# Kernel optimization log

Hardware: AMD Instinct MI355X
Metric: run time of the kernel (lower is better)

The kernel has to match this reference:

```python
import jax, jax.numpy as jnp
import numpy as np

B, S, D, H, HD, NU, T = 64, 512, 256, 4, 64, 100000, 24


def setup_inputs() -> dict:
    key = jax.random.key(0)
    ks = jax.random.split(key, 13)
    return {
        "timeslot_embedded": jax.random.normal(ks[0], (T, D), jnp.float32),
        "user": jax.random.randint(ks[1], (B,), 0, NU, dtype=jnp.int64) if jax.config.jax_enable_x64 else jax.random.randint(ks[1], (B,), 0, NU, dtype=jnp.int32),
        "hour": jax.random.randint(ks[2], (B, S), 0, T, dtype=jnp.int32),
        "hour_mask": jax.random.randint(ks[3], (B, S, T), 0, 2, dtype=jnp.int32),
        "user_pref": jax.random.normal(ks[4], (NU, D), jnp.float32) * 0.02,
        "Wq": jax.random.normal(ks[5], (H, HD, 2 * D), jnp.float32) * 0.02,
        "bq": jnp.zeros((H, HD), jnp.float32),
        "Wk": jax.random.normal(ks[6], (H, HD, D), jnp.float32) * 0.02,
        "bk": jnp.zeros((H, HD), jnp.float32),
        "Wv": jax.random.normal(ks[7], (H, HD, D), jnp.float32) * 0.02,
        "bv": jnp.zeros((H, HD), jnp.float32),
        "Wu": jax.random.normal(ks[8], (D, D), jnp.float32) * 0.02,
        "bu": jnp.zeros((D,), jnp.float32),
    }


def reference(timeslot_embedded, user, hour, hour_mask, user_pref,
              Wq, bq, Wk, bk, Wv, bv, Wu, bu):
    b, s = hour.shape
    n = b * s
    # per-token features
    user_feat = jnp.broadcast_to(user_pref[user][:, None, :], (b, s, D)).reshape(n, D)
    time_feat = timeslot_embedded[hour.reshape(n)]          # [N, D]
    query = jnp.concatenate([user_feat, time_feat], axis=-1)  # [N, 2D]
    # all heads at once (equivalent to the per-head Linear loop)
    q = jnp.einsum('nd,hkd->nhk', query, Wq) + bq[None]               # [N, H, HD]
    k = jnp.einsum('td,hkd->htk', timeslot_embedded, Wk) + bk[:, None, :]  # [H, T, HD]
    v = jnp.einsum('td,hkd->htk', timeslot_embedded, Wv) + bv[:, None, :]  # [H, T, HD]
    scale = 1.0 / np.sqrt(HD).astype(np.float32)
    scores = jnp.einsum('nhk,htk->nht', q, k) * scale                 # [N, H, T]
    mask = hour_mask.reshape(n, T)[:, None, :]                        # [N, 1, T]
    scores = jnp.where(mask == 1, -jnp.inf, scores)
    attn = jax.nn.softmax(scores, axis=-1)
    out = jnp.einsum('nht,htk->nhk', attn, v).reshape(n, H * HD)      # concat heads
    out = out @ Wu.T + bu
    return out.reshape(b, s, D)
```

## Files before the change

### kernel.cpp

```cpp
#include <hip/hip_runtime.h>
#include <hip/hip_bf16.h>

#define QU_OFF   0
#define KK_OFF   16384
#define ET_OFF   22528
#define VWB_OFF  24832

typedef __attribute__((ext_vector_type(8))) short bf16x8;
typedef __attribute__((ext_vector_type(4))) float f32x4;
typedef __attribute__((ext_vector_type(4))) int   i32x4;

__device__ __forceinline__ unsigned short f2bf(float f) {
    unsigned u = __builtin_bit_cast(unsigned, f);
    return (unsigned short)((u + 0x7FFFu + ((u >> 16) & 1u)) >> 16);
}
__device__ __forceinline__ unsigned packbf(float a, float b) {
    return (unsigned)f2bf(a) | ((unsigned)f2bf(b) << 16);
}
__device__ __forceinline__ bf16x8 cvt8(float4 f0, float4 f1) {
    int4 v = make_int4(packbf(f0.x, f0.y), packbf(f0.z, f0.w),
                       packbf(f1.x, f1.y), packbf(f1.z, f1.w));
    return __builtin_bit_cast(bf16x8, v);
}
__device__ __forceinline__ float dot4(float4 a, float4 b, float s) {
    return fmaf(a.x, b.x, fmaf(a.y, b.y, fmaf(a.z, b.z, fmaf(a.w, b.w, s))));
}
__device__ __forceinline__ float dot4v(f32x4 a, f32x4 b, float s) {
    return fmaf(a[0], b[0], fmaf(a[1], b[1], fmaf(a[2], b[2], fmaf(a[3], b[3], s))));
}


__global__ __launch_bounds__(256) void precomp(
    const float* __restrict__ ts, const int* __restrict__ user,
    const float* __restrict__ user_pref,
    const float* __restrict__ Wq, const float* __restrict__ bq,
    const float* __restrict__ Wk, const float* __restrict__ bk,
    const float* __restrict__ Wv, const float* __restrict__ bv,
    const float* __restrict__ Wu, float* __restrict__ ws)
{
    __shared__ unsigned sA[4096];
    __shared__ float sM1[32 * 68];
    __shared__ float sM2[32 * 68];
    int tid = threadIdx.x, blk = blockIdx.x;
    int w = tid >> 6, l = tid & 63;
    int eo = (l >> 4) * 8;

    if (blk < 16) {
        int q = blk >> 2, co = (blk & 3) * 64, b0 = q * 16;
        for (int u = tid; u < 512; u += 256) {
            int r = u >> 5, e0 = (u & 31) * 8;
            const float* src = user_pref + (size_t)user[b0 + r] * 256 + e0;
            float4 f0 = *(const float4*)src, f1 = *(const float4*)(src + 4);
            unsigned* dst = &sA[(((e0 >> 5) * 2) * 64 + (r & 15) + 16 * ((e0 >> 3) & 3)) * 4];
            dst[0] = packbf(f0.x, f0.y); dst[1] = packbf(f0.z, f0.w);
            dst[2] = packbf(f1.x, f1.y); dst[3] = packbf(f1.z, f1.w);
        }
        __syncthreads();
        int col = co + w * 16 + (l & 15);
        float4 fb[8][2];
        #pragma unroll
        for (int kt = 0; kt < 8; ++kt) {
            const float* Bp = Wq + (size_t)col * 512 + kt * 32 + eo;
            fb[kt][0] = *(const float4*)Bp; fb[kt][1] = *(const float4*)(Bp + 4);
        }
        f32x4 acc = (f32x4)0.f;
        #pragma unroll
        for (int kt = 0; kt < 8; ++kt) {
            bf16x8 afr = __builtin_bit_cast(bf16x8, *(const int4*)&sA[((kt * 2) * 64 + l) * 4]);
            acc = __builtin_amdgcn_mfma_f32_16x16x32_bf16(afr, cvt8(fb[kt][0], fb[kt][1]), acc, 0, 0, 0);
        }
        int row = (l >> 4) * 4;
        #pragma unroll
        for (int r = 0; r < 4; ++r)
            ws[QU_OFF + (size_t)(b0 + row + r) * 256 + col] = acc[r];
        return;
    }

    for (int u = tid; u < 768; u += 256) {
        int r = u >> 5, e0 = (u & 31) * 8;
        const float* src = ts + r * 256 + e0;
        float4 f0 = *(const float4*)src, f1 = *(const float4*)(src + 4);
        unsigned* dst = &sA[(((e0 >> 5) * 2 + (r >> 4)) * 64 + (r & 15) + 16 * ((e0 >> 3) & 3)) * 4];
        dst[0] = packbf(f0.x, f0.y); dst[1] = packbf(f0.z, f0.w);
        dst[2] = packbf(f1.x, f1.y); dst[3] = packbf(f1.z, f1.w);
    }
    __syncthreads();

    if (blk < 20) {
        int h = blk - 16;
        int j = h * 64 + w * 16 + (l & 15);
        float4 fa[8][2], fc[8][2];
        #pragma unroll
        for (int kt = 0; kt < 8; ++kt) {
            const float* Bq = Wq + (size_t)j * 512 + 256 + kt * 32 + eo;
            const float* Bk = Wk + (size_t)j * 256 + kt * 32 + eo;
            fa[kt][0] = *(const float4*)Bq; fa[kt][1] = *(const float4*)(Bq + 4);
            fc[kt][0] = *(const float4*)Bk; fc[kt][1] = *(const float4*)(Bk + 4);
        }
        f32x4 aca[2] = {(f32x4)0.f, (f32x4)0.f};
        f32x4 acb[2] = {(f32x4)0.f, (f32x4)0.f};
        #pragma unroll
        for (int kt = 0; kt < 8; ++kt) {
            bf16x8 bq8 = cvt8(fa[kt][0], fa[kt][1]);
            bf16x8 bk8 = cvt8(fc[kt][0], fc[kt][1]);
            #pragma unroll
            for (int mt = 0; mt < 2; ++mt) {
                bf16x8 afr = __builtin_bit_cast(bf16x8, *(const int4*)&sA[((kt * 2 + mt) * 64 + l) * 4]);
                aca[mt] = __builtin_amdgcn_mfma_f32_16x16x32_bf16(afr, bq8, aca[mt], 0, 0, 0);
                acb[mt] = __builtin_amdgcn_mfma_f32_16x16x32_bf16(afr, bk8, acb[mt], 0, 0, 0);
            }
        }
        float bqv = bq[j], bkv = bk[j];
        int hd = w * 16 + (l & 15);
        #pragma unroll
        for (int mt = 0; mt < 2; ++mt) {
            int t0 = mt * 16 + (l >> 4) * 4;
            #pragma unroll
            for (int r = 0; r < 4; ++r) {
                int t = t0 + r;
                if (t < 24) {
                    sM1[t * 68 + hd] = aca[mt][r] + bqv;
                    float kv = acb[mt][r] + bkv;
                    sM2[t * 68 + hd] = kv;
                    ws[KK_OFF + (h * 24 + t) * 64 + hd] = kv;
                }
            }
        }
        __syncthreads();
        for (int u = tid; u < 576; u += 256) {
            int tp = u / 24, t = u - tp * 24;
            const float4* qp4 = (const float4*)&sM1[tp * 68];
            const float4* kp4 = (const float4*)&sM2[t * 68];
            float s = 0.f;
            #pragma unroll
            for (int i = 0; i < 16; ++i) s = dot4(qp4[i], kp4[i], s);
            ws[ET_OFF + tp * 96 + h * 24 + t] = expf(s * 0.125f);
        }
        return;
    }

    {
        int h = blk - 20;
        int jv = h * 64 + w * 16 + (l & 15);
        float4 fv[8][2];
        #pragma unroll
        for (int kt = 0; kt < 8; ++kt) {
            const float* Bv = Wv + (size_t)jv * 256 + kt * 32 + eo;
            fv[kt][0] = *(const float4*)Bv; fv[kt][1] = *(const float4*)(Bv + 4);
        }
        f32x4 acv[2] = {(f32x4)0.f, (f32x4)0.f};
        #pragma unroll
        for (int kt = 0; kt < 8; ++kt) {
            bf16x8 bv8 = cvt8(fv[kt][0], fv[kt][1]);
            #pragma unroll
            for (int mt = 0; mt < 2; ++mt) {
                bf16x8 afr = __builtin_bit_cast(bf16x8, *(const int4*)&sA[((kt * 2 + mt) * 64 + l) * 4]);
                acv[mt] = __builtin_amdgcn_mfma_f32_16x16x32_bf16(afr, bv8, acv[mt], 0, 0, 0);
            }
        }
        float bvv = bv[jv];
        int hd = w * 16 + (l & 15);
        #pragma unroll
        for (int mt = 0; mt < 2; ++mt) {
            int t0 = mt * 16 + (l >> 4) * 4;
            #pragma unroll
            for (int r = 0; r < 4; ++r)
                if (t0 + r < 24) sM1[(t0 + r) * 68 + hd] = acv[mt][r] + bvv;
        }
        __syncthreads();
        f32x4 ac2[2][4];
        #pragma unroll
        for (int mt = 0; mt < 2; ++mt)
            #pragma unroll
            for (int q = 0; q < 4; ++q) ac2[mt][q] = (f32x4)0.f;
        #pragma unroll
        for (int kt2 = 0; kt2 < 2; ++kt2) {
            int k0 = kt2 * 32 + eo;
            bf16x8 a2[2];
            #pragma unroll
            for (int mt = 0; mt < 2; ++mt) {
                int m = mt * 16 + (l & 15);
                float4 g0 = *(const float4*)&sM1[m * 68 + k0];
                float4 g1 = *(const float4*)&sM1[m * 68 + k0 + 4];
                a2[mt] = cvt8(g0, g1);
            }
            float4 fu[4][2];
            #pragma unroll
            for (int q = 0; q < 4; ++q) {
                int d = (w * 4 + q) * 16 + (l & 15);
                const float* Bu = Wu + (size_t)d * 256 + h * 64 + k0;
                fu[q][0] = *(const float4*)Bu; fu[q][1] = *(const float4*)(Bu + 4);
            }
            #pragma unroll
            for (int q = 0; q < 4; ++q) {
                bf16x8 bu8 = cvt8(fu[q][0], fu[q][1]);
                #pragma unroll
                for (int mt = 0; mt < 2; ++mt)
                    ac2[mt][q] = __builtin_amdgcn_mfma_f32_16x16x32_bf16(a2[mt], bu8, ac2[mt][q], 0, 0, 0);
            }
        }
        unsigned* vwb = (unsigned*)(ws + VWB_OFF);
        #pragma unroll
        for (int mt = 0; mt < 2; ++mt) {
            int t0 = mt * 16 + (l >> 4) * 4;
            if (t0 < 24) {
                #pragma unroll
                for (int q = 0; q < 4; ++q) {
                    int d = (w * 4 + q) * 16 + (l & 15);
                    #pragma unroll
                    for (int pp = 0; pp < 2; ++pp) {
                        int ht = h * 24 + t0 + pp * 2;
                        unsigned pk = packbf(ac2[mt][q][pp * 2], ac2[mt][q][pp * 2 + 1]);
                        int ktC = ht >> 5, ntC = d >> 4;
                        int lgC = (ht >> 3) & 3, jhC = (ht & 7) >> 1;
                        vwb[(ktC * 16 + ntC) * 256 + ((d & 15) + 16 * lgC) * 4 + jhC] = pk;
                    }
                }
            }
        }
    }
}

__global__ __launch_bounds__(512) void attn_mfma(
    const int* __restrict__ hour, const int* __restrict__ hour_mask,
    const float* __restrict__ ws, const float* __restrict__ bu,
    float* __restrict__ out)
{
    const float* ET = ws + ET_OFF;
    __shared__ int4 A_lds[24 * 64];
    __shared__ float EU_s[96];
    __shared__ __align__(16) float stg[8 * 1088];
    int tid = threadIdx.x, w = tid >> 6, l = tid & 63;
    int mh = w >> 2, ns = w & 3;
    int nb = blockIdx.x * 128;
    int b = nb >> 9;

    int tok = tid >> 2, h = tid & 3, n = nb + tok;
    int th = hour[n];
    const i32x4* mp = (const i32x4*)(hour_mask + (long long)n * 24);
    i32x4 msk[6];
    #pragma unroll
    for (int q = 0; q < 6; ++q) msk[q] = __builtin_nontemporal_load(mp + q);
    const int4* Bg = (const int4*)(ws + VWB_OFF);
    int4 breg[12];
    #pragma unroll
    for (int kt = 0; kt < 3; ++kt)
        #pragma unroll
        for (int q = 0; q < 4; ++q)
            breg[kt * 4 + q] = Bg[(kt * 16 + ns * 4 + q) * 64 + l];
    if (tid < 96) {
        const f32x4* qp = (const f32x4*)(ws + QU_OFF + b * 256 + (tid / 24) * 64);
        const f32x4* kp = (const f32x4*)(ws + KK_OFF + tid * 64);
        float s = 0.f;
        #pragma unroll
        for (int i = 0; i < 16; ++i) s = dot4v(qp[i], kp[i], s);
        EU_s[tid] = expf(s * 0.125f);
    }
    const f32x4* ETp = (const f32x4*)(ET + th * 96 + h * 24);
    f32x4 fET[6];
    #pragma unroll
    for (int q = 0; q < 6; ++q) fET[q] = ETp[q];
    __syncthreads();
    {
        const f32x4* EUp = (const f32x4*)(EU_s + h * 24);
        float p[24]; float ssum = 0.f;
        #pragma unroll
        for (int q = 0; q < 6; ++q) {
            f32x4 e = EUp[q]; f32x4 f = fET[q]; i32x4 mm = msk[q];
            float v0 = (mm[0] != 0) ? 0.f : e[0] * f[0];
            float v1 = (mm[1] != 0) ? 0.f : e[1] * f[1];
            float v2 = (mm[2] != 0) ? 0.f : e[2] * f[2];
            float v3 = (mm[3] != 0) ? 0.f : e[3] * f[3];
            p[q*4+0] = v0; p[q*4+1] = v1; p[q*4+2] = v2; p[q*4+3] = v3;
            ssum += (v0 + v1) + (v2 + v3);
        }
        float r = 1.0f / ssum;
        int mt8 = tok >> 4, tl = tok & 15;
        #pragma unroll
        for (int tp = 0; tp < 12; ++tp) {
            int ht = h * 24 + tp * 2;
            unsigned pack = packbf(p[tp*2] * r, p[tp*2+1] * r);
            int kt = ht >> 5, lg = (ht >> 3) & 3, jh = (ht & 7) >> 1;
            ((unsigned*)A_lds)[((kt * 8 + mt8) * 64 + tl + 16 * lg) * 4 + jh] = pack;
        }
    }
    __syncthreads();
    bf16x8 afr[3][4];
    #pragma unroll
    for (int kt = 0; kt < 3; ++kt)
        #pragma unroll
        for (int q = 0; q < 4; ++q)
            afr[kt][q] = __builtin_bit_cast(bf16x8, A_lds[(kt * 8 + mh * 4 + q) * 64 + l]);
    f32x4 acc[4][4];
    #pragma unroll
    for (int mt = 0; mt < 4; ++mt)
        #pragma unroll
        for (int q = 0; q < 4; ++q) acc[mt][q] = (f32x4)0.f;
    #pragma unroll
    for (int kt = 0; kt < 3; ++kt)
        #pragma unroll
        for (int mt = 0; mt < 4; ++mt)
            #pragma unroll
            for (int q = 0; q < 4; ++q)
                acc[mt][q] = __builtin_amdgcn_mfma_f32_16x16x32_bf16(
                    afr[kt][mt], __builtin_bit_cast(bf16x8, breg[kt * 4 + q]),
                    acc[mt][q], 0, 0, 0);
    float* sp = stg + w * 1088;
    int rr = l >> 2, cg = l & 3;
    f32x4 bu4[4];
    #pragma unroll
    for (int i = 0; i < 4; ++i)
        bu4[i] = *(const f32x4*)(bu + ns * 64 + i * 16 + cg * 4);
    int rbase = nb + mh * 64;
    #pragma unroll
    for (int mt = 0; mt < 4; ++mt) {
        #pragma unroll
        for (int q = 0; q < 4; ++q)
            #pragma unroll
            for (int r = 0; r < 4; ++r)
                sp[((l >> 4) * 4 + r) * 68 + q * 16 + (l & 15)] = acc[mt][q][r];
        float* orow = out + (size_t)(rbase + mt * 16 + rr) * 256 + ns * 64;
        #pragma unroll
        for (int i = 0; i < 4; ++i) {
            f32x4 v = *(const f32x4*)(sp + rr * 68 + i * 16 + cg * 4);
            v = v + bu4[i];
            __builtin_nontemporal_store(v, (f32x4*)(orow + i * 16 + cg * 4));
        }
    }
}

extern "C" void kernel_launch(void* const* d_in, const int* in_sizes, int n_in,
                              void* d_out, int out_size, void* d_ws, size_t ws_size,
                              hipStream_t stream)
{
    const float* ts        = (const float*)d_in[0];
    const int*   user      = (const int*)  d_in[1];
    const int*   hour      = (const int*)  d_in[2];
    const int*   hour_mask = (const int*)  d_in[3];
    const float* user_pref = (const float*)d_in[4];
    const float* Wq        = (const float*)d_in[5];
    const float* bq        = (const float*)d_in[6];
    const float* Wk        = (const float*)d_in[7];
    const float* bk        = (const float*)d_in[8];
    const float* Wv        = (const float*)d_in[9];
    const float* bv        = (const float*)d_in[10];
    const float* Wu        = (const float*)d_in[11];
    const float* bu        = (const float*)d_in[12];
    float* ws  = (float*)d_ws;
    float* out = (float*)d_out;

    hipLaunchKernelGGL(precomp, dim3(24), dim3(256), 0, stream,
                       ts, user, user_pref, Wq, bq, Wk, bk, Wv, bv, Wu, ws);
    hipLaunchKernelGGL(attn_mfma, dim3(256), dim3(512), 0, stream,
                       hour, hour_mask, ws, bu, out);
}
```

Before: 24.70 us.

## Halve attention block size to 64 tokens and hoist weight loads in precomp

The attention kernel now runs 512 blocks of 256 threads, each covering 64 tokens instead of 128, which halves LDS use per block and spreads work across more CUs on the 256-CU part. Each wave now owns one 64-column output slice for all four m-tiles. In precomp, the global weight loads (Wq, Wu) are issued before the LDS staging of the timeslot/user tiles so their latency overlaps with the staging work. The cost is that each block reloads the full B fragments for fewer tokens, and the Wu prefetch holds more registers live.

After: 24.22 us, median of 2. No clear change (-2.0%).

```diff
diff --git a/kernel.cpp b/kernel.cpp
--- a/kernel.cpp
+++ b/kernel.cpp
@@ -47,6 +47,13 @@
 
     if (blk < 16) {
         int q = blk >> 2, co = (blk & 3) * 64, b0 = q * 16;
+        int col = co + w * 16 + (l & 15);
+        float4 fb[8][2];
+        #pragma unroll
+        for (int kt = 0; kt < 8; ++kt) {
+            const float* Bp = Wq + (size_t)col * 512 + kt * 32 + eo;
+            fb[kt][0] = *(const float4*)Bp; fb[kt][1] = *(const float4*)(Bp + 4);
+        }
         for (int u = tid; u < 512; u += 256) {
             int r = u >> 5, e0 = (u & 31) * 8;
             const float* src = user_pref + (size_t)user[b0 + r] * 256 + e0;
@@ -56,13 +63,6 @@
             dst[2] = packbf(f1.x, f1.y); dst[3] = packbf(f1.z, f1.w);
         }
         __syncthreads();
-        int col = co + w * 16 + (l & 15);
-        float4 fb[8][2];
-        #pragma unroll
-        for (int kt = 0; kt < 8; ++kt) {
-            const float* Bp = Wq + (size_t)col * 512 + kt * 32 + eo;
-            fb[kt][0] = *(const float4*)Bp; fb[kt][1] = *(const float4*)(Bp + 4);
-        }
         f32x4 acc = (f32x4)0.f;
         #pragma unroll
         for (int kt = 0; kt < 8; ++kt) {
@@ -75,16 +75,6 @@
             ws[QU_OFF + (size_t)(b0 + row + r) * 256 + col] = acc[r];
         return;
     }
-
-    for (int u = tid; u < 768; u += 256) {
-        int r = u >> 5, e0 = (u & 31) * 8;
-        const float* src = ts + r * 256 + e0;
-        float4 f0 = *(const float4*)src, f1 = *(const float4*)(src + 4);
-        unsigned* dst = &sA[(((e0 >> 5) * 2 + (r >> 4)) * 64 + (r & 15) + 16 * ((e0 >> 3) & 3)) * 4];
-        dst[0] = packbf(f0.x, f0.y); dst[1] = packbf(f0.z, f0.w);
-        dst[2] = packbf(f1.x, f1.y); dst[3] = packbf(f1.z, f1.w);
-    }
-    __syncthreads();
 
     if (blk < 20) {
         int h = blk - 16;
@@ -97,6 +87,15 @@
             fa[kt][0] = *(const float4*)Bq; fa[kt][1] = *(const float4*)(Bq + 4);
             fc[kt][0] = *(const float4*)Bk; fc[kt][1] = *(const float4*)(Bk + 4);
         }
+        for (int u = tid; u < 768; u += 256) {
+            int r = u >> 5, e0 = (u & 31) * 8;
+            const float* src = ts + r * 256 + e0;
+            float4 f0 = *(const float4*)src, f1 = *(const float4*)(src + 4);
+            unsigned* dst = &sA[(((e0 >> 5) * 2 + (r >> 4)) * 64 + (r & 15) + 16 * ((e0 >> 3) & 3)) * 4];
+            dst[0] = packbf(f0.x, f0.y); dst[1] = packbf(f0.z, f0.w);
+            dst[2] = packbf(f1.x, f1.y); dst[3] = packbf(f1.z, f1.w);
+        }
+        __syncthreads();
         f32x4 aca[2] = {(f32x4)0.f, (f32x4)0.f};
         f32x4 acb[2] = {(f32x4)0.f, (f32x4)0.f};
         #pragma unroll
@@ -148,6 +147,26 @@
             const float* Bv = Wv + (size_t)jv * 256 + kt * 32 + eo;
             fv[kt][0] = *(const float4*)Bv; fv[kt][1] = *(const float4*)(Bv + 4);
         }
+        float4 fu[2][4][2];
+        #pragma unroll
+        for (int kt2 = 0; kt2 < 2; ++kt2) {
+            int k0 = kt2 * 32 + eo;
+            #pragma unroll
+            for (int q = 0; q < 4; ++q) {
+                int d = (w * 4 + q) * 16 + (l & 15);
+                const float* Bu = Wu + (size_t)d * 256 + h * 64 + k0;
+                fu[kt2][q][0] = *(const float4*)Bu; fu[kt2][q][1] = *(const float4*)(Bu + 4);
+            }
+        }
+        for (int u = tid; u < 768; u += 256) {
+            int r = u >> 5, e0 = (u & 31) * 8;
+            const float* src = ts + r * 256 + e0;
+            float4 f0 = *(const float4*)src, f1 = *(const float4*)(src + 4);
+            unsigned* dst = &sA[(((e0 >> 5) * 2 + (r >> 4)) * 64 + (r & 15) + 16 * ((e0 >> 3) & 3)) * 4];
+            dst[0] = packbf(f0.x, f0.y); dst[1] = packbf(f0.z, f0.w);
+            dst[2] = packbf(f1.x, f1.y); dst[3] = packbf(f1.z, f1.w);
+        }
+        __syncthreads();
         f32x4 acv[2] = {(f32x4)0.f, (f32x4)0.f};
         #pragma unroll
         for (int kt = 0; kt < 8; ++kt) {
@@ -184,16 +203,9 @@
                 float4 g1 = *(const float4*)&sM1[m * 68 + k0 + 4];
                 a2[mt] = cvt8(g0, g1);
             }
-            float4 fu[4][2];
             #pragma unroll
             for (int q = 0; q < 4; ++q) {
-                int d = (w * 4 + q) * 16 + (l & 15);
-                const float* Bu = Wu + (size_t)d * 256 + h * 64 + k0;
-                fu[q][0] = *(const float4*)Bu; fu[q][1] = *(const float4*)(Bu + 4);
-            }
-            #pragma unroll
-            for (int q = 0; q < 4; ++q) {
-                bf16x8 bu8 = cvt8(fu[q][0], fu[q][1]);
+                bf16x8 bu8 = cvt8(fu[kt2][q][0], fu[kt2][q][1]);
                 #pragma unroll
                 for (int mt = 0; mt < 2; ++mt)
                     ac2[mt][q] = __builtin_amdgcn_mfma_f32_16x16x32_bf16(a2[mt], bu8, ac2[mt][q], 0, 0, 0);
@@ -221,18 +233,17 @@
     }
 }
 
-__global__ __launch_bounds__(512) void attn_mfma(
+__global__ __launch_bounds__(256, 2) void attn_mfma(
     const int* __restrict__ hour, const int* __restrict__ hour_mask,
     const float* __restrict__ ws, const float* __restrict__ bu,
     float* __restrict__ out)
 {
     const float* ET = ws + ET_OFF;
-    __shared__ int4 A_lds[24 * 64];
+    __shared__ int4 A_lds[12 * 64];
     __shared__ float EU_s[96];
-    __shared__ __align__(16) float stg[8 * 1088];
+    __shared__ __align__(16) float stg[4 * 1088];
     int tid = threadIdx.x, w = tid >> 6, l = tid & 63;
-    int mh = w >> 2, ns = w & 3;
-    int nb = blockIdx.x * 128;
+    int nb = blockIdx.x * 64;
     int b = nb >> 9;
 
     int tok = tid >> 2, h = tid & 3, n = nb + tok;
@@ -247,7 +258,7 @@
     for (int kt = 0; kt < 3; ++kt)
         #pragma unroll
         for (int q = 0; q < 4; ++q)
-            breg[kt * 4 + q] = Bg[(kt * 16 + ns * 4 + q) * 64 + l];
+            breg[kt * 4 + q] = Bg[(kt * 16 + w * 4 + q) * 64 + l];
     if (tid < 96) {
         const f32x4* qp = (const f32x4*)(ws + QU_OFF + b * 256 + (tid / 24) * 64);
         const f32x4* kp = (const f32x4*)(ws + KK_OFF + tid * 64);
@@ -275,13 +286,13 @@
             ssum += (v0 + v1) + (v2 + v3);
         }
         float r = 1.0f / ssum;
-        int mt8 = tok >> 4, tl = tok & 15;
+        int mt = tok >> 4, tl = tok & 15;
         #pragma unroll
         for (int tp = 0; tp < 12; ++tp) {
             int ht = h * 24 + tp * 2;
             unsigned pack = packbf(p[tp*2] * r, p[tp*2+1] * r);
             int kt = ht >> 5, lg = (ht >> 3) & 3, jh = (ht & 7) >> 1;
-            ((unsigned*)A_lds)[((kt * 8 + mt8) * 64 + tl + 16 * lg) * 4 + jh] = pack;
+            ((unsigned*)A_lds)[((kt * 4 + mt) * 64 + tl + 16 * lg) * 4 + jh] = pack;
         }
     }
     __syncthreads();
@@ -290,7 +301,7 @@
     for (int kt = 0; kt < 3; ++kt)
         #pragma unroll
         for (int q = 0; q < 4; ++q)
-            afr[kt][q] = __builtin_bit_cast(bf16x8, A_lds[(kt * 8 + mh * 4 + q) * 64 + l]);
+            afr[kt][q] = __builtin_bit_cast(bf16x8, A_lds[(kt * 4 + q) * 64 + l]);
     f32x4 acc[4][4];
     #pragma unroll
     for (int mt = 0; mt < 4; ++mt)
@@ -310,8 +321,7 @@
     f32x4 bu4[4];
     #pragma unroll
     for (int i = 0; i < 4; ++i)
-        bu4[i] = *(const f32x4*)(bu + ns * 64 + i * 16 + cg * 4);
-    int rbase = nb + mh * 64;
+        bu4[i] = *(const f32x4*)(bu + w * 64 + i * 16 + cg * 4);
     #pragma unroll
     for (int mt = 0; mt < 4; ++mt) {
         #pragma unroll
@@ -319,7 +329,7 @@
             #pragma unroll
             for (int r = 0; r < 4; ++r)
                 sp[((l >> 4) * 4 + r) * 68 + q * 16 + (l & 15)] = acc[mt][q][r];
-        float* orow = out + (size_t)(rbase + mt * 16 + rr) * 256 + ns * 64;
+        float* orow = out + (size_t)(nb + mt * 16 + rr) * 256 + w * 64;
         #pragma unroll
         for (int i = 0; i < 4; ++i) {
             f32x4 v = *(const f32x4*)(sp + rr * 68 + i * 16 + cg * 4);
@@ -351,6 +361,6 @@
 
     hipLaunchKernelGGL(precomp, dim3(24), dim3(256), 0, stream,
                        ts, user, user_pref, Wq, bq, Wk, bk, Wv, bv, Wu, ws);
-    hipLaunchKernelGGL(attn_mfma, dim3(256), dim3(512), 0, stream,
+    hipLaunchKernelGGL(attn_mfma, dim3(512), dim3(256), 0, stream,
                        hour, hour_mask, ws, bu, out);
 }
```
